# Optimization experiments

Measured on AMD Instinct MI355X. Metric: run time of the kernel, lower is better.

The kernel has to match this reference:

```python
import jax, jax.numpy as jnp
import numpy as np

NUM_STEPS = 3  # matches init_kwargs num_steps
UNITS = 256
N_STRUCT = 4096
N_ATOMS_TOTAL = 131072
FEAT_IN = 256


def setup_inputs() -> dict:
    key = jax.random.key(0)
    ks = jax.random.split(key, 7)
    field = jax.random.normal(ks[0], (N_ATOMS_TOTAL, FEAT_IN), dtype=jnp.float32)
    # Dense(units) params
    Wd = jax.random.normal(ks[1], (FEAT_IN, UNITS), dtype=jnp.float32) / np.sqrt(FEAT_IN)
    bd = jnp.zeros((UNITS,), dtype=jnp.float32)
    # Keras LSTM params: kernel [2*units, 4*units], recurrent [units, 4*units], bias [4*units]
    Wk = jax.random.normal(ks[2], (2 * UNITS, 4 * UNITS), dtype=jnp.float32) / np.sqrt(2 * UNITS)
    Wr = jax.random.normal(ks[3], (UNITS, 4 * UNITS), dtype=jnp.float32) / np.sqrt(UNITS)
    b_lstm = jnp.zeros((4 * UNITS,), dtype=jnp.float32)
    # sorted segment ids = get_segment_indices_from_n(counts)
    segment_ids = jnp.sort(jax.random.randint(ks[4], (N_ATOMS_TOTAL,), 0, N_STRUCT)).astype(jnp.int32)
    return {"field": field, "Wd": Wd, "bd": bd, "Wk": Wk, "Wr": Wr,
            "b_lstm": b_lstm, "segment_ids": segment_ids, "n_struct": N_STRUCT}


def _segment_softmax(e, seg, num_segments):
    # per-channel softmax within each segment (matches unsorted_segment_softmax)
    m = jax.ops.segment_max(e, seg, num_segments=num_segments)
    ex = jnp.exp(e - m[seg])
    s = jax.ops.segment_sum(ex, seg, num_segments=num_segments)
    return ex / s[seg]


def _lstm_step(x, h, c, Wk, Wr, b):
    # Keras gate order: i, f, g(c), o
    z = x @ Wk + h @ Wr + b
    i, f, g, o = jnp.split(z, 4, axis=-1)
    c_new = jax.nn.sigmoid(f) * c + jax.nn.sigmoid(i) * jnp.tanh(g)
    h_new = jax.nn.sigmoid(o) * jnp.tanh(c_new)
    return h_new, c_new


def reference(field, Wd, bd, Wk, Wr, b_lstm, segment_ids, n_struct):
    units = Wd.shape[1]
    x = field @ Wd + bd                              # [N_atoms, units]
    q_star = jnp.zeros((n_struct, 2 * units), dtype=x.dtype)
    h = jnp.zeros((n_struct, units), dtype=x.dtype)
    c = jnp.zeros((n_struct, units), dtype=x.dtype)
    for _ in range(NUM_STEPS):
        h, c = _lstm_step(q_star, h, c, Wk, Wr, b_lstm)
        qt = h                                        # [n_struct, units]
        eit = x * qt[segment_ids]                     # gather == tf.repeat(qt, counts)
        ait = _segment_softmax(eit, segment_ids, n_struct)
        rt = jax.ops.segment_sum(ait * x, segment_ids, num_segments=n_struct)
        q_star = jnp.concatenate([qt, rt], axis=-1)   # [n_struct, 2*units]
    return q_star
```

## Files before the change

kernel.cpp:

```cpp
#include <hip/hip_runtime.h>
#include <math.h>

#define N_ATOMS   131072
#define FEAT      256
#define UNITS     256
#define NSTRUCT   4096
#define ZDIM      1024
#define QDIM      512
#define KLSTM     512
#define LDP       40

typedef __attribute__((ext_vector_type(8))) __bf16 bf16x8;
typedef __attribute__((ext_vector_type(4))) float  f32x4;

__device__ __forceinline__ float sigm(float v) { return 1.0f / (1.0f + __expf(-v)); }

__device__ __forceinline__ unsigned short bf16_rne(float v) {
    unsigned int u = __float_as_uint(v);
    u += 0x7fffu + ((u >> 16) & 1u);
    return (unsigned short)(u >> 16);
}
__device__ __forceinline__ float bf16_f32(unsigned short b) {
    return __uint_as_float(((unsigned int)b) << 16);
}
__device__ __forceinline__ bf16x8 frag_ld(const unsigned short* p) {
    uint4 u = *(const uint4*)p;
    bf16x8 r; __builtin_memcpy(&r, &u, 16); return r;
}
__device__ __forceinline__ void gload16(const unsigned short* g, unsigned short* l) {
    __builtin_amdgcn_global_load_lds(
        (const __attribute__((address_space(1))) unsigned int*)g,
        (__attribute__((address_space(3))) unsigned int*)l, 16, 0, 0);
}

__global__ void seg_offs_kernel(const int* __restrict__ seg, int* __restrict__ offs) {
    int s = blockIdx.x * blockDim.x + threadIdx.x;
    if (s > NSTRUCT) return;
    int lo = 0, hi = N_ATOMS;
    while (lo < hi) {
        int mid = (lo + hi) >> 1;
        if (seg[mid] < s) lo = mid + 1; else hi = mid;
    }
    offs[s] = lo;
}

__global__ __launch_bounds__(256) void prep_wd_kernel(
    const float* __restrict__ Wd, unsigned short* __restrict__ Th,
    unsigned short* __restrict__ Tl)
{
    int t = blockIdx.x * 256 + threadIdx.x;
    int k = t >> 8, n = t & 255;
    float v = Wd[t];
    unsigned short h = bf16_rne(v);
    unsigned short l = bf16_rne(v - bf16_f32(h));
    Th[n * FEAT + k] = h;
    Tl[n * FEAT + k] = l;
}

__global__ __launch_bounds__(256) void prep_wlstm_kernel(
    const float* __restrict__ Wk, const float* __restrict__ Wr,
    unsigned short* __restrict__ Th, unsigned short* __restrict__ Tl)
{
    int t = blockIdx.x * 256 + threadIdx.x;
    int k = t >> 10, n = t & 1023;
    float v = Wk[(size_t)k * ZDIM + n];
    if (k < 256) v += Wr[(size_t)k * ZDIM + n];
    unsigned short h = bf16_rne(v);
    unsigned short l = bf16_rne(v - bf16_f32(h));
    Th[(size_t)n * KLSTM + k] = h;
    Tl[(size_t)n * KLSTM + k] = l;
}

__global__ __launch_bounds__(256) void gemm_split(
    const float* __restrict__ A, int lda, int K,
    const unsigned short* __restrict__ BTh,
    const unsigned short* __restrict__ BTl,
    const float* __restrict__ bias, float* __restrict__ C, int ldc)
{
    __shared__ unsigned short Ah[128][LDP], Al[128][LDP];
    __shared__ unsigned short Bh[128 * 32], Bl[128 * 32];
    const int bn = blockIdx.x * 128;
    const int bm = blockIdx.y * 128;
    const int t  = threadIdx.x;
    const int w  = t >> 6, l = t & 63;
    const int wr = w & 1, wc = w >> 1;
    const int lm = l & 15, koff = (l >> 4) * 8;

    f32x4 acc[4][4] = {};
    float4 pa[4];

    #pragma unroll
    for (int i = 0; i < 2; ++i) {
        int flat = t + i * 256;
        int n = flat >> 2, kc = flat & 3;
        gload16(&BTh[(size_t)(bn + n) * K + kc * 8], &Bh[(size_t)(w * 64 + i * 256) * 8]);
        gload16(&BTl[(size_t)(bn + n) * K + kc * 8], &Bl[(size_t)(w * 64 + i * 256) * 8]);
    }
    #pragma unroll
    for (int i = 0; i < 4; ++i) {
        int flat = t + i * 256;
        int m = flat >> 3, kq = flat & 7;
        pa[i] = *(const float4*)&A[(size_t)(bm + m) * lda + kq * 4];
    }

    for (int k0 = 0; k0 < K; k0 += 32) {
        #pragma unroll
        for (int i = 0; i < 4; ++i) {
            int flat = t + i * 256;
            int m = flat >> 3, kq = flat & 7;
            float4 v = pa[i];
            unsigned short h0 = bf16_rne(v.x), h1 = bf16_rne(v.y);
            unsigned short h2 = bf16_rne(v.z), h3 = bf16_rne(v.w);
            unsigned short l0 = bf16_rne(v.x - bf16_f32(h0));
            unsigned short l1 = bf16_rne(v.y - bf16_f32(h1));
            unsigned short l2 = bf16_rne(v.z - bf16_f32(h2));
            unsigned short l3 = bf16_rne(v.w - bf16_f32(h3));
            uint2 hw, lw;
            hw.x = (unsigned)h0 | ((unsigned)h1 << 16);
            hw.y = (unsigned)h2 | ((unsigned)h3 << 16);
            lw.x = (unsigned)l0 | ((unsigned)l1 << 16);
            lw.y = (unsigned)l2 | ((unsigned)l3 << 16);
            *(uint2*)&Ah[m][kq * 4] = hw;
            *(uint2*)&Al[m][kq * 4] = lw;
        }
        __syncthreads();

        const bool more = (k0 + 32) < K;
        if (more) {
            #pragma unroll
            for (int i = 0; i < 4; ++i) {
                int flat = t + i * 256;
                int m = flat >> 3, kq = flat & 7;
                pa[i] = *(const float4*)&A[(size_t)(bm + m) * lda + k0 + 32 + kq * 4];
            }
        }

        bf16x8 ah[4], al[4];
        #pragma unroll
        for (int i = 0; i < 4; ++i) {
            ah[i] = frag_ld(&Ah[wr * 64 + i * 16 + lm][koff]);
            al[i] = frag_ld(&Al[wr * 64 + i * 16 + lm][koff]);
        }
        #pragma unroll
        for (int j = 0; j < 4; ++j) {
            bf16x8 bh = frag_ld(&Bh[(size_t)(wc * 64 + j * 16 + lm) * 32 + koff]);
            bf16x8 bl = frag_ld(&Bl[(size_t)(wc * 64 + j * 16 + lm) * 32 + koff]);
            #pragma unroll
            for (int i = 0; i < 4; ++i) {
                acc[i][j] = __builtin_amdgcn_mfma_f32_16x16x32_bf16(ah[i], bh, acc[i][j], 0, 0, 0);
                acc[i][j] = __builtin_amdgcn_mfma_f32_16x16x32_bf16(al[i], bh, acc[i][j], 0, 0, 0);
                acc[i][j] = __builtin_amdgcn_mfma_f32_16x16x32_bf16(ah[i], bl, acc[i][j], 0, 0, 0);
            }
        }
        __syncthreads();
        if (more) {
            #pragma unroll
            for (int i = 0; i < 2; ++i) {
                int flat = t + i * 256;
                int n = flat >> 2, kc = flat & 3;
                gload16(&BTh[(size_t)(bn + n) * K + k0 + 32 + kc * 8],
                        &Bh[(size_t)(w * 64 + i * 256) * 8]);
                gload16(&BTl[(size_t)(bn + n) * K + k0 + 32 + kc * 8],
                        &Bl[(size_t)(w * 64 + i * 256) * 8]);
            }
        }
    }

    const int lg4 = (l >> 4) * 4;
    #pragma unroll
    for (int i = 0; i < 4; ++i)
        #pragma unroll
        for (int j = 0; j < 4; ++j) {
            int col  = bn + wc * 64 + j * 16 + lm;
            int row0 = bm + wr * 64 + i * 16 + lg4;
            float bb = bias[col];
            #pragma unroll
            for (int r = 0; r < 4; ++r)
                C[(size_t)(row0 + r) * ldc + col] = acc[i][j][r] + bb;
        }
}

__global__ __launch_bounds__(1024) void attn_fused(
    const float* __restrict__ x, const float* __restrict__ zsrc, int use_z,
    float* __restrict__ c, const int* __restrict__ offs,
    float* __restrict__ qstar_out)
{
    __shared__ float hq[UNITS];
    __shared__ float Lm[4][UNITS], Ls[4][UNITS], Lr[4][UNITS];
    const int s  = blockIdx.x;
    const int t  = threadIdx.x;
    const int ch = t & 255;
    const int p  = t >> 8;

    if (p == 0) {
        float zi, zf, zg, zo, cold;
        if (use_z) {
            const float* zr = zsrc + (size_t)s * ZDIM;
            zi = zr[ch]; zf = zr[256 + ch]; zg = zr[512 + ch]; zo = zr[768 + ch];
            cold = c[(size_t)s * UNITS + ch];
        } else {
            zi = zsrc[ch]; zf = zsrc[256 + ch]; zg = zsrc[512 + ch]; zo = zsrc[768 + ch];
            cold = 0.0f;
        }
        float cn = sigm(zf) * cold + sigm(zi) * tanhf(zg);
        float hn = sigm(zo) * tanhf(cn);
        c[(size_t)s * UNITS + ch] = cn;
        hq[ch] = hn;
    }
    __syncthreads();

    const float q = hq[ch];
    const int a0 = offs[s], a1 = offs[s + 1];

    float m = -INFINITY, ssum = 0.0f, r = 0.0f;
    int a = a0 + p;
    for (; a + 12 < a1; a += 16) {
        float x0 = x[(size_t)(a +  0) * FEAT + ch];
        float x1 = x[(size_t)(a +  4) * FEAT + ch];
        float x2 = x[(size_t)(a +  8) * FEAT + ch];
        float x3 = x[(size_t)(a + 12) * FEAT + ch];
        float e0 = x0 * q, e1 = x1 * q, e2 = x2 * q, e3 = x3 * q;
        float mn = fmaxf(fmaxf(fmaxf(e0, e1), fmaxf(e2, e3)), m);
        float sc = __expf(m - mn);
        float p0 = __expf(e0 - mn), p1 = __expf(e1 - mn);
        float p2 = __expf(e2 - mn), p3 = __expf(e3 - mn);
        ssum = ssum * sc + ((p0 + p1) + (p2 + p3));
        r    = r    * sc + ((p0 * x0 + p1 * x1) + (p2 * x2 + p3 * x3));
        m = mn;
    }
    for (; a < a1; a += 4) {
        float xv = x[(size_t)a * FEAT + ch];
        float e = xv * q;
        float mn = fmaxf(m, e);
        float sc = __expf(m - mn);
        float pe = __expf(e - mn);
        ssum = ssum * sc + pe;
        r = r * sc + pe * xv;
        m = mn;
    }
    Lm[p][ch] = m; Ls[p][ch] = ssum; Lr[p][ch] = r;
    __syncthreads();

    if (p == 0) {
        float m0 = Lm[0][ch], m1 = Lm[1][ch], m2 = Lm[2][ch], m3 = Lm[3][ch];
        float ms = fmaxf(fmaxf(m0, m1), fmaxf(m2, m3));
        float rt = 0.0f;
        if (a1 > a0) {
            float w0 = __expf(m0 - ms), w1 = __expf(m1 - ms);
            float w2 = __expf(m2 - ms), w3 = __expf(m3 - ms);
            float S = Ls[0][ch] * w0 + Ls[1][ch] * w1 + Ls[2][ch] * w2 + Ls[3][ch] * w3;
            float R = Lr[0][ch] * w0 + Lr[1][ch] * w1 + Lr[2][ch] * w2 + Lr[3][ch] * w3;
            rt = R / S;
        }
        qstar_out[(size_t)s * QDIM + ch] = q;
        qstar_out[(size_t)s * QDIM + UNITS + ch] = rt;
    }
}

extern "C" void kernel_launch(void* const* d_in, const int* in_sizes, int n_in,
                              void* d_out, int out_size, void* d_ws, size_t ws_size,
                              hipStream_t stream) {
    const float* field  = (const float*)d_in[0];
    const float* Wd     = (const float*)d_in[1];
    const float* bd     = (const float*)d_in[2];
    const float* Wk     = (const float*)d_in[3];
    const float* Wr     = (const float*)d_in[4];
    const float* b_lstm = (const float*)d_in[5];
    const int*   segids = (const int*)d_in[6];

    float* ws   = (float*)d_ws;
    float* x    = ws;
    float* z    = x + (size_t)N_ATOMS * FEAT;
    float* qst  = z + (size_t)NSTRUCT * ZDIM;
    float* c    = qst + (size_t)NSTRUCT * QDIM;
    int*   offs = (int*)(c + (size_t)NSTRUCT * UNITS);

    unsigned short* wdt_h = (unsigned short*)d_out;
    unsigned short* wdt_l = wdt_h + 256 * 256;
    unsigned short* wt_h  = wdt_l + 256 * 256;
    unsigned short* wt_l  = wt_h + (size_t)ZDIM * KLSTM;

    seg_offs_kernel<<<(NSTRUCT + 1 + 255) / 256, 256, 0, stream>>>(segids, offs);
    prep_wd_kernel<<<256, 256, 0, stream>>>(Wd, wdt_h, wdt_l);
    prep_wlstm_kernel<<<ZDIM * KLSTM / 256, 256, 0, stream>>>(Wk, Wr, wt_h, wt_l);

    gemm_split<<<dim3(FEAT / 128, N_ATOMS / 128), 256, 0, stream>>>(
        field, FEAT, FEAT, wdt_h, wdt_l, bd, x, FEAT);

    attn_fused<<<NSTRUCT, 1024, 0, stream>>>(x, b_lstm, 0, c, offs, qst);

    for (int step = 1; step < 3; ++step) {
        gemm_split<<<dim3(ZDIM / 128, NSTRUCT / 128), 256, 0, stream>>>(
            qst, KLSTM, KLSTM, wt_h, wt_l, b_lstm, z, ZDIM);
        float* qdst = (step == 2) ? (float*)d_out : qst;
        attn_fused<<<NSTRUCT, 1024, 0, stream>>>(x, z, 1, c, offs, qdst);
    }
}
```

Before: 413.7 us.

## Use one thread per channel with 8 independent softmax accumulators

The attention kernel shrinks from 1024 threads per block (4 atom-partitions per channel merged through shared memory) to 256 threads per block. Each thread walks all atoms of its segment and keeps 8 independent online-softmax accumulators, which it merges at the end. This drops the shared-memory merge and the two block barriers and gives each thread more independent loads in flight. In exchange, each block has fewer threads to hide memory latency, and per-thread register use goes up.

```diff
diff --git a/kernel.cpp b/kernel.cpp
--- a/kernel.cpp
+++ b/kernel.cpp
@@ -180,81 +180,75 @@
         }
 }
 
-__global__ __launch_bounds__(1024) void attn_fused(
+__global__ __launch_bounds__(256) void attn_fused(
     const float* __restrict__ x, const float* __restrict__ zsrc, int use_z,
     float* __restrict__ c, const int* __restrict__ offs,
     float* __restrict__ qstar_out)
 {
-    __shared__ float hq[UNITS];
-    __shared__ float Lm[4][UNITS], Ls[4][UNITS], Lr[4][UNITS];
     const int s  = blockIdx.x;
-    const int t  = threadIdx.x;
-    const int ch = t & 255;
-    const int p  = t >> 8;
-
-    if (p == 0) {
-        float zi, zf, zg, zo, cold;
-        if (use_z) {
-            const float* zr = zsrc + (size_t)s * ZDIM;
-            zi = zr[ch]; zf = zr[256 + ch]; zg = zr[512 + ch]; zo = zr[768 + ch];
-            cold = c[(size_t)s * UNITS + ch];
-        } else {
-            zi = zsrc[ch]; zf = zsrc[256 + ch]; zg = zsrc[512 + ch]; zo = zsrc[768 + ch];
-            cold = 0.0f;
-        }
-        float cn = sigm(zf) * cold + sigm(zi) * tanhf(zg);
-        float hn = sigm(zo) * tanhf(cn);
-        c[(size_t)s * UNITS + ch] = cn;
-        hq[ch] = hn;
-    }
-    __syncthreads();
-
-    const float q = hq[ch];
+    const int ch = threadIdx.x;
+
+    float zi, zf, zg, zo, cold;
+    if (use_z) {
+        const float* zr = zsrc + (size_t)s * ZDIM;
+        zi = zr[ch]; zf = zr[256 + ch]; zg = zr[512 + ch]; zo = zr[768 + ch];
+        cold = c[(size_t)s * UNITS + ch];
+    } else {
+        zi = zsrc[ch]; zf = zsrc[256 + ch]; zg = zsrc[512 + ch]; zo = zsrc[768 + ch];
+        cold = 0.0f;
+    }
+    float cn = sigm(zf) * cold + sigm(zi) * tanhf(zg);
+    float q  = sigm(zo) * tanhf(cn);
+    c[(size_t)s * UNITS + ch] = cn;
+
     const int a0 = offs[s], a1 = offs[s + 1];
-
-    float m = -INFINITY, ssum = 0.0f, r = 0.0f;
-    int a = a0 + p;
-    for (; a + 12 < a1; a += 16) {
-        float x0 = x[(size_t)(a +  0) * FEAT + ch];
-        float x1 = x[(size_t)(a +  4) * FEAT + ch];
-        float x2 = x[(size_t)(a +  8) * FEAT + ch];
-        float x3 = x[(size_t)(a + 12) * FEAT + ch];
-        float e0 = x0 * q, e1 = x1 * q, e2 = x2 * q, e3 = x3 * q;
-        float mn = fmaxf(fmaxf(fmaxf(e0, e1), fmaxf(e2, e3)), m);
-        float sc = __expf(m - mn);
-        float p0 = __expf(e0 - mn), p1 = __expf(e1 - mn);
-        float p2 = __expf(e2 - mn), p3 = __expf(e3 - mn);
-        ssum = ssum * sc + ((p0 + p1) + (p2 + p3));
-        r    = r    * sc + ((p0 * x0 + p1 * x1) + (p2 * x2 + p3 * x3));
-        m = mn;
-    }
-    for (; a < a1; a += 4) {
+    float m[8], ss[8], rr[8];
+    #pragma unroll
+    for (int j = 0; j < 8; ++j) { m[j] = -INFINITY; ss[j] = 0.0f; rr[j] = 0.0f; }
+
+    int a = a0;
+    for (; a + 7 < a1; a += 8) {
+        float xv[8];
+        #pragma unroll
+        for (int j = 0; j < 8; ++j) xv[j] = x[(size_t)(a + j) * FEAT + ch];
+        #pragma unroll
+        for (int j = 0; j < 8; ++j) {
+            float e  = xv[j] * q;
+            float mn = fmaxf(m[j], e);
+            float sc = __expf(m[j] - mn);
+            float pe = __expf(e - mn);
+            ss[j] = ss[j] * sc + pe;
+            rr[j] = rr[j] * sc + pe * xv[j];
+            m[j] = mn;
+        }
+    }
+    for (; a < a1; ++a) {
         float xv = x[(size_t)a * FEAT + ch];
-        float e = xv * q;
-        float mn = fmaxf(m, e);
-        float sc = __expf(m - mn);
+        float e  = xv * q;
+        float mn = fmaxf(m[0], e);
+        float sc = __expf(m[0] - mn);
         float pe = __expf(e - mn);
-        ssum = ssum * sc + pe;
-        r = r * sc + pe * xv;
-        m = mn;
-    }
-    Lm[p][ch] = m; Ls[p][ch] = ssum; Lr[p][ch] = r;
-    __syncthreads();
-
-    if (p == 0) {
-        float m0 = Lm[0][ch], m1 = Lm[1][ch], m2 = Lm[2][ch], m3 = Lm[3][ch];
-        float ms = fmaxf(fmaxf(m0, m1), fmaxf(m2, m3));
-        float rt = 0.0f;
-        if (a1 > a0) {
-            float w0 = __expf(m0 - ms), w1 = __expf(m1 - ms);
-            float w2 = __expf(m2 - ms), w3 = __expf(m3 - ms);
-            float S = Ls[0][ch] * w0 + Ls[1][ch] * w1 + Ls[2][ch] * w2 + Ls[3][ch] * w3;
-            float R = Lr[0][ch] * w0 + Lr[1][ch] * w1 + Lr[2][ch] * w2 + Lr[3][ch] * w3;
-            rt = R / S;
-        }
-        qstar_out[(size_t)s * QDIM + ch] = q;
-        qstar_out[(size_t)s * QDIM + UNITS + ch] = rt;
-    }
+        ss[0] = ss[0] * sc + pe;
+        rr[0] = rr[0] * sc + pe * xv;
+        m[0] = mn;
+    }
+
+    float rt = 0.0f;
+    if (a1 > a0) {
+        float ms = m[0];
+        #pragma unroll
+        for (int j = 1; j < 8; ++j) ms = fmaxf(ms, m[j]);
+        float S = 0.0f, R = 0.0f;
+        #pragma unroll
+        for (int j = 0; j < 8; ++j) {
+            float wj = __expf(m[j] - ms);
+            S += ss[j] * wj;
+            R += rr[j] * wj;
+        }
+        rt = R / S;
+    }
+    qstar_out[(size_t)s * QDIM + ch] = q;
+    qstar_out[(size_t)s * QDIM + UNITS + ch] = rt;
 }
 
 extern "C" void kernel_launch(void* const* d_in, const int* in_sizes, int n_in,
@@ -287,12 +281,12 @@
     gemm_split<<<dim3(FEAT / 128, N_ATOMS / 128), 256, 0, stream>>>(
         field, FEAT, FEAT, wdt_h, wdt_l, bd, x, FEAT);
 
-    attn_fused<<<NSTRUCT, 1024, 0, stream>>>(x, b_lstm, 0, c, offs, qst);
+    attn_fused<<<NSTRUCT, 256, 0, stream>>>(x, b_lstm, 0, c, offs, qst);
 
     for (int step = 1; step < 3; ++step) {
         gemm_split<<<dim3(ZDIM / 128, NSTRUCT / 128), 256, 0, stream>>>(
             qst, KLSTM, KLSTM, wt_h, wt_l, b_lstm, z, ZDIM);
         float* qdst = (step == 2) ? (float*)d_out : qst;
-        attn_fused<<<NSTRUCT, 1024, 0, stream>>>(x, z, 1, c, offs, qdst);
-    }
-}
+        attn_fused<<<NSTRUCT, 256, 0, stream>>>(x, z, 1, c, offs, qdst);
+    }
+}
```

New measurement: 407.8 us. Within noise of the previous version (-1.4%).
